# Kernel optimization log

Hardware: AMD Instinct MI355X
Metric: run time of the kernel (lower is better)

The kernel has to match this reference:

```python
import jax, jax.numpy as jnp
import numpy as np

N = 10000
E = 160000
H = 8
C = 128
D = 1024
NB = 3
NG = 64
NEG_SLOPE = 0.2
BN_EPS = 1e-5


def setup_inputs() -> dict:
    key = jax.random.key(0)
    ks = jax.random.split(key, 12)
    x = jax.random.normal(ks[0], (N, D), dtype=jnp.float32)
    edge_index = jax.random.randint(ks[1], (2, E), 0, N, dtype=jnp.int64)
    batch = jnp.sort(jax.random.randint(ks[2], (N,), 0, NG, dtype=jnp.int64))
    W = jax.random.normal(ks[3], (NB, D, D), dtype=jnp.float32) * 0.03
    att_src = jax.random.normal(ks[4], (NB, H, C), dtype=jnp.float32) * 0.1
    att_dst = jax.random.normal(ks[5], (NB, H, C), dtype=jnp.float32) * 0.1
    att_bias = jnp.zeros((NB, D), dtype=jnp.float32)
    gamma = jnp.ones((NB, D), dtype=jnp.float32)
    beta = jnp.zeros((NB, D), dtype=jnp.float32)
    W_out = jax.random.normal(ks[6], (D, 2), dtype=jnp.float32) * 0.03
    b_out = jnp.zeros((2,), dtype=jnp.float32)
    return {"x": x, "edge_index": edge_index, "batch": batch, "W": W,
            "att_src": att_src, "att_dst": att_dst, "att_bias": att_bias,
            "gamma": gamma, "beta": beta, "W_out": W_out, "b_out": b_out}


def _gat_conv(x, Wb, a_src, a_dst, bias, src, dst):
    # linear projection, per-head view: [N, H, C]
    h = (x @ Wb).reshape(N, H, C)
    alpha_src = jnp.einsum('nhc,hc->nh', h, a_src)  # [N,H]
    alpha_dst = jnp.einsum('nhc,hc->nh', h, a_dst)
    e = jax.nn.leaky_relu(alpha_src[src] + alpha_dst[dst], NEG_SLOPE)  # [Etot,H]
    # segment softmax over incoming edges per destination node
    m = jax.ops.segment_max(e, dst, num_segments=N)  # every node has self-loop
    ex = jnp.exp(e - m[dst])
    denom = jax.ops.segment_sum(ex, dst, num_segments=N)
    alpha = ex / denom[dst]  # [Etot,H]
    msg = alpha[:, :, None] * h[src]  # [Etot,H,C]
    out = jax.ops.segment_sum(msg, dst, num_segments=N).reshape(N, H * C)
    return out + bias


def _batchnorm(x, g, b):
    mu = jnp.mean(x, axis=0)
    var = jnp.mean(jnp.square(x - mu), axis=0)  # biased, training mode
    return (x - mu) * jax.lax.rsqrt(var + BN_EPS) * g + b


def reference(x, edge_index, batch, W, att_src, att_dst, att_bias, gamma, beta, W_out, b_out):
    # add self loops (PyG GATConv default)
    loop = jnp.arange(N, dtype=edge_index.dtype)
    src = jnp.concatenate([edge_index[0], loop])
    dst = jnp.concatenate([edge_index[1], loop])

    h = x
    prev = x
    for i in range(NB):
        att = _gat_conv(h, W[i], att_src[i], att_dst[i], att_bias[i], src, dst)
        o = jax.nn.relu(_batchnorm(prev + att, gamma[i], beta[i]))
        prev = h
        h = o

    # global mean pool over graphs
    sums = jax.ops.segment_sum(h, batch, num_segments=NG)
    cnts = jax.ops.segment_sum(jnp.ones((N,), dtype=h.dtype), batch, num_segments=NG)
    pooled = sums / jnp.maximum(cnts, 1.0)[:, None]
    return pooled @ W_out + b_out
```

## Files before the change

kernel.cpp:

```cpp
#include <hip/hip_runtime.h>
#include <hip/hip_bf16.h>

#define N_NODES 10000
#define E_EDGES 160000
#define ETOT    170000
#define H_HEADS 8
#define C_CH    128
#define D_DIM   1024
#define NBLK    3
#define NGRAPH  64
#define NEG_SLOPE 0.2f
#define BN_EPS  1e-5f

typedef __attribute__((ext_vector_type(8))) _Float16 half8;
typedef __attribute__((ext_vector_type(4))) _Float16 half4;
typedef __attribute__((ext_vector_type(2))) _Float16 half2v;
typedef __attribute__((ext_vector_type(4))) float f32x4;

__device__ inline int lower_bound_batch(const int* __restrict__ batch, int g) {
    int lo = 0, hi = N_NODES;
    while (lo < hi) {
        int mid = (lo + hi) >> 1;
        if (batch[mid] < g) lo = mid + 1;
        else hi = mid;
    }
    return lo;
}

__global__ void deg_kernel(const int* __restrict__ ei, int* __restrict__ deg) {
    int tid = blockIdx.x * blockDim.x + threadIdx.x;
    if (tid >= ETOT) return;
    int dst = (tid < E_EDGES) ? ei[E_EDGES + tid] : (tid - E_EDGES);
    atomicAdd(&deg[dst], 1);
}

__global__ void scan_kernel(const int* __restrict__ deg, int* __restrict__ ioff) {
    __shared__ int part[256];
    int t = threadIdx.x;
    const int CH = (N_NODES + 255) / 256;
    int base = t * CH;
    int s = 0;
    for (int j = 0; j < CH; ++j) {
        int idx = base + j;
        if (idx < N_NODES) s += deg[idx];
    }
    part[t] = s;
    __syncthreads();
    for (int o = 1; o < 256; o <<= 1) {
        int v = 0;
        if (t >= o) v = part[t - o];
        __syncthreads();
        part[t] += v;
        __syncthreads();
    }
    int run = (t == 0) ? 0 : part[t - 1];
    for (int j = 0; j < CH; ++j) {
        int idx = base + j;
        if (idx < N_NODES) { ioff[idx] = run; run += deg[idx]; }
    }
}

__global__ void scatter_kernel(const int* __restrict__ ei, int* __restrict__ ioff,
                               int* __restrict__ csr_src) {
    int tid = blockIdx.x * blockDim.x + threadIdx.x;
    if (tid >= ETOT) return;
    int src, dst;
    if (tid < E_EDGES) { src = ei[tid]; dst = ei[E_EDGES + tid]; }
    else { src = dst = tid - E_EDGES; }
    int pos = atomicAdd(&ioff[dst], 1);
    csr_src[pos] = src;
}

__global__ __launch_bounds__(256) void xconv_kernel(const float* __restrict__ in,
                                                    _Float16* __restrict__ o, int n4) {
    int i = blockIdx.x * blockDim.x + threadIdx.x;
    if (i >= n4) return;
    float4 v = ((const float4*)in)[i];
    half4 h = {(_Float16)v.x, (_Float16)v.y, (_Float16)v.z, (_Float16)v.w};
    ((half4*)o)[i] = h;
}

__global__ __launch_bounds__(256) void wtconv_kernel(const float* __restrict__ Wall,
                                                     _Float16* __restrict__ t16all) {
    const float* W = Wall + (size_t)blockIdx.z * D_DIM * D_DIM;
    _Float16* t16 = t16all + (size_t)blockIdx.z * D_DIM * D_DIM;
    __shared__ float t[32][33];
    int bn = blockIdx.x * 32;
    int bk = blockIdx.y * 32;
    int tx = threadIdx.x & 31;
    int ty = threadIdx.x >> 5;
#pragma unroll
    for (int r = 0; r < 32; r += 8)
        t[ty + r][tx] = W[(size_t)(bk + ty + r) * D_DIM + bn + tx];
    __syncthreads();
#pragma unroll
    for (int r = 0; r < 32; r += 8)
        t16[(size_t)(bn + ty + r) * D_DIM + bk + tx] = (_Float16)t[tx][ty + r];
}

__global__ __launch_bounds__(256) void gemm_mfma_kernel(const _Float16* __restrict__ A,
                                                        const _Float16* __restrict__ Bt,
                                                        _Float16* __restrict__ Hout,
                                                        const float* __restrict__ att_s,
                                                        const float* __restrict__ att_d,
                                                        float* __restrict__ asrc,
                                                        float* __restrict__ adst, int M) {
    __shared__ short As[128 * 32];
    __shared__ short Bs[128 * 32];
    __shared__ float sA[128], sD[128];
    int bm = blockIdx.y * 128;
    int bn = blockIdx.x * 128;
    int head = blockIdx.x;
    int tid = threadIdx.x;
    int wave = tid >> 6;
    int lane = tid & 63;
    int wm = (wave >> 1) * 64;
    int wn = (wave & 1) * 64;
    int quad = lane >> 4;
    int l16 = lane & 15;

    f32x4 acc[4][4];
#pragma unroll
    for (int i = 0; i < 4; ++i)
#pragma unroll
        for (int j = 0; j < 4; ++j) acc[i][j] = (f32x4){0.f, 0.f, 0.f, 0.f};

    int srow = lane >> 2;
    int scol = (lane & 3) * 16;

    for (int kb = 0; kb < 32; ++kb) {
        int k0 = kb * 32;
#pragma unroll
        for (int r = 0; r < 2; ++r) {
            int arow = wave * 16 + r * 64 + srow;
            int grow = bm + arow;
            if (grow > M - 1) grow = M - 1;
            const char* gp = (const char*)(A + (size_t)grow * 1024 + k0) + scol;
            __builtin_amdgcn_global_load_lds(
                (const __attribute__((address_space(1))) void*)gp,
                (__attribute__((address_space(3))) void*)((char*)As + (wave * 16 + r * 64) * 64),
                16, 0, 0);
        }
#pragma unroll
        for (int r = 0; r < 2; ++r) {
            int brow = wave * 16 + r * 64 + srow;
            const char* gp = (const char*)(Bt + (size_t)(bn + brow) * 1024 + k0) + scol;
            __builtin_amdgcn_global_load_lds(
                (const __attribute__((address_space(1))) void*)gp,
                (__attribute__((address_space(3))) void*)((char*)Bs + (wave * 16 + r * 64) * 64),
                16, 0, 0);
        }
        __syncthreads();

        half8 af[4], bfr[4];
#pragma unroll
        for (int i = 0; i < 4; ++i)
            af[i] = *(const half8*)(As + (wm + i * 16 + l16) * 32 + quad * 8);
#pragma unroll
        for (int j = 0; j < 4; ++j)
            bfr[j] = *(const half8*)(Bs + (wn + j * 16 + l16) * 32 + quad * 8);
#pragma unroll
        for (int i = 0; i < 4; ++i)
#pragma unroll
            for (int j = 0; j < 4; ++j)
                acc[i][j] = __builtin_amdgcn_mfma_f32_16x16x32_f16(af[i], bfr[j], acc[i][j], 0, 0, 0);
        __syncthreads();
    }

    float wsv[4], wdv[4];
#pragma unroll
    for (int j = 0; j < 4; ++j) {
        int c = wn + j * 16 + l16;
        wsv[j] = att_s[head * 128 + c];
        wdv[j] = att_d[head * 128 + c];
    }
    float psv[4][4], pdv[4][4];
#pragma unroll
    for (int i = 0; i < 4; ++i) {
#pragma unroll
        for (int reg = 0; reg < 4; ++reg) {
            float p = acc[i][0][reg] * wsv[0] + acc[i][1][reg] * wsv[1] +
                      acc[i][2][reg] * wsv[2] + acc[i][3][reg] * wsv[3];
            float q = acc[i][0][reg] * wdv[0] + acc[i][1][reg] * wdv[1] +
                      acc[i][2][reg] * wdv[2] + acc[i][3][reg] * wdv[3];
#pragma unroll
            for (int o = 1; o < 16; o <<= 1) {
                p += __shfl_xor(p, o);
                q += __shfl_xor(q, o);
            }
            psv[i][reg] = p;
            pdv[i][reg] = q;
        }
    }
    if ((wave & 1) == 0 && l16 == 0) {
#pragma unroll
        for (int i = 0; i < 4; ++i)
#pragma unroll
            for (int reg = 0; reg < 4; ++reg) {
                int r = wm + i * 16 + quad * 4 + reg;
                sA[r] = psv[i][reg];
                sD[r] = pdv[i][reg];
            }
    }
#pragma unroll
    for (int i = 0; i < 4; ++i) {
#pragma unroll
        for (int reg = 0; reg < 4; ++reg) {
            int gr = bm + wm + i * 16 + quad * 4 + reg;
            if (gr < M) {
                _Float16* hp = Hout + (size_t)head * N_NODES * 128 + (size_t)gr * 128 + wn + l16;
#pragma unroll
                for (int j = 0; j < 4; ++j) hp[j * 16] = (_Float16)acc[i][j][reg];
            }
        }
    }
    __syncthreads();
    if ((wave & 1) == 1 && l16 == 0) {
#pragma unroll
        for (int i = 0; i < 4; ++i)
#pragma unroll
            for (int reg = 0; reg < 4; ++reg) {
                int r = wm + i * 16 + quad * 4 + reg;
                int gr = bm + r;
                if (gr < M) {
                    asrc[gr * 8 + head] = sA[r] + psv[i][reg];
                    adst[gr * 8 + head] = sD[r] + pdv[i][reg];
                }
            }
    }
}

__global__ __launch_bounds__(256) void agg_kernel(const _Float16* __restrict__ h16,
                                                  const float* __restrict__ asrc,
                                                  const float* __restrict__ adst,
                                                  const int* __restrict__ ioff,
                                                  const int* __restrict__ csr_src,
                                                  const _Float16* __restrict__ prevh,
                                                  const float* __restrict__ bias,
                                                  _Float16* __restrict__ yout,
                                                  float* __restrict__ stats) {
    int bx = blockIdx.x;
    int tid = threadIdx.x;
    if (bx == 0) {
#pragma unroll
        for (int j = 0; j < 8; ++j) stats[tid + j * 256] = 0.f;
    }
    int head = bx & 7;
    int chunk = bx >> 3;
    int sub = tid >> 5;
    int lane = tid & 31;
    int n = chunk * 8 + sub;
    int c4 = lane * 4;
    const _Float16* hh = h16 + (size_t)head * N_NODES * 128;
    int start = (n == 0) ? 0 : ioff[n - 1];
    int end = ioff[n];
    float ad = adst[n * 8 + head];
    float den = 0.f;
    float4 acc = make_float4(0.f, 0.f, 0.f, 0.f);
    int p = start;
    for (; p + 4 <= end; p += 4) {
        int s0 = csr_src[p + 0];
        int s1 = csr_src[p + 1];
        int s2 = csr_src[p + 2];
        int s3 = csr_src[p + 3];
        float a0 = asrc[s0 * 8 + head];
        float a1 = asrc[s1 * 8 + head];
        float a2 = asrc[s2 * 8 + head];
        float a3 = asrc[s3 * 8 + head];
        half4 h0 = *(const half4*)(hh + (size_t)s0 * 128 + c4);
        half4 h1 = *(const half4*)(hh + (size_t)s1 * 128 + c4);
        half4 h2 = *(const half4*)(hh + (size_t)s2 * 128 + c4);
        half4 h3 = *(const half4*)(hh + (size_t)s3 * 128 + c4);
        float e0 = a0 + ad; e0 = (e0 > 0.f) ? e0 : NEG_SLOPE * e0;
        float e1 = a1 + ad; e1 = (e1 > 0.f) ? e1 : NEG_SLOPE * e1;
        float e2 = a2 + ad; e2 = (e2 > 0.f) ? e2 : NEG_SLOPE * e2;
        float e3 = a3 + ad; e3 = (e3 > 0.f) ? e3 : NEG_SLOPE * e3;
        float x0 = __expf(e0), x1 = __expf(e1), x2 = __expf(e2), x3 = __expf(e3);
        den += (x0 + x1) + (x2 + x3);
        acc.x += x0 * (float)h0[0] + x1 * (float)h1[0] + x2 * (float)h2[0] + x3 * (float)h3[0];
        acc.y += x0 * (float)h0[1] + x1 * (float)h1[1] + x2 * (float)h2[1] + x3 * (float)h3[1];
        acc.z += x0 * (float)h0[2] + x1 * (float)h1[2] + x2 * (float)h2[2] + x3 * (float)h3[2];
        acc.w += x0 * (float)h0[3] + x1 * (float)h1[3] + x2 * (float)h2[3] + x3 * (float)h3[3];
    }
    for (; p < end; ++p) {
        int s = csr_src[p];
        float e = asrc[s * 8 + head] + ad;
        e = (e > 0.f) ? e : NEG_SLOPE * e;
        float ex = __expf(e);
        den += ex;
        half4 hv = *(const half4*)(hh + (size_t)s * 128 + c4);
        acc.x = fmaf(ex, (float)hv[0], acc.x);
        acc.y = fmaf(ex, (float)hv[1], acc.y);
        acc.z = fmaf(ex, (float)hv[2], acc.z);
        acc.w = fmaf(ex, (float)hv[3], acc.w);
    }
    float invd = 1.0f / den;
    int col = head * 128 + c4;
    half4 ph = *(const half4*)(prevh + (size_t)n * 1024 + col);
    float4 bv = *(const float4*)(bias + col);
    float r0 = fmaf(acc.x, invd, (float)ph[0] + bv.x);
    float r1 = fmaf(acc.y, invd, (float)ph[1] + bv.y);
    float r2 = fmaf(acc.z, invd, (float)ph[2] + bv.z);
    float r3 = fmaf(acc.w, invd, (float)ph[3] + bv.w);
    half4 o = {(_Float16)r0, (_Float16)r1, (_Float16)r2, (_Float16)r3};
    *(half4*)(yout + (size_t)n * 1024 + col) = o;
}

__global__ void bn_stats_kernel(const _Float16* __restrict__ y, float* __restrict__ stats) {
    int col = (blockIdx.x * 256 + threadIdx.x) * 2;
    float s0 = 0.f, s1 = 0.f, q0 = 0.f, q1 = 0.f;
    for (int r = blockIdx.y; r < N_NODES; r += gridDim.y) {
        half2v v = *(const half2v*)(y + (size_t)r * 1024 + col);
        float a = (float)v[0], b = (float)v[1];
        s0 += a; q0 += a * a;
        s1 += b; q1 += b * b;
    }
    atomicAdd(&stats[col], s0);
    atomicAdd(&stats[col + 1], s1);
    atomicAdd(&stats[1024 + col], q0);
    atomicAdd(&stats[1024 + col + 1], q1);
}

__global__ void bn_apply_kernel(const _Float16* __restrict__ y, const float* __restrict__ stats,
                                const float* __restrict__ gamma, const float* __restrict__ beta,
                                _Float16* __restrict__ oout) {
    int idx4 = blockIdx.x * blockDim.x + threadIdx.x;
    if (idx4 >= N_NODES * D_DIM / 4) return;
    int base = idx4 * 4;
    int col = base & 1023;
    const float invN = 1.0f / (float)N_NODES;
    half4 v = ((const half4*)y)[idx4];
    float r[4];
#pragma unroll
    for (int j = 0; j < 4; ++j) {
        int cc = col + j;
        float mu = stats[cc] * invN;
        float var = stats[1024 + cc] * invN - mu * mu;
        float t = ((float)v[j] - mu) * rsqrtf(var + BN_EPS) * gamma[cc] + beta[cc];
        r[j] = fmaxf(t, 0.f);
    }
    half4 h = {(_Float16)r[0], (_Float16)r[1], (_Float16)r[2], (_Float16)r[3]};
    ((half4*)oout)[idx4] = h;
}

__global__ __launch_bounds__(256) void pool_kernel(const _Float16* __restrict__ h3,
                                                   const int* __restrict__ batch,
                                                   float* __restrict__ pooled) {
    int col = blockIdx.x * 256 + threadIdx.x;
    int g = blockIdx.y;
    int lo = lower_bound_batch(batch, g);
    int hi = lower_bound_batch(batch, g + 1);
    float acc = 0.f;
    for (int r = lo; r < hi; ++r) acc += (float)h3[(size_t)r * 1024 + col];
    pooled[(size_t)g * 1024 + col] = acc;
}

__global__ void final_kernel(const float* __restrict__ pooled, const int* __restrict__ batch,
                             const float* __restrict__ Wout, const float* __restrict__ bout,
                             float* __restrict__ out) {
    int g = blockIdx.x;
    int t = threadIdx.x;
    float p0 = 0.f, p1 = 0.f;
    for (int d = t; d < 1024; d += 256) {
        float v = pooled[(size_t)g * 1024 + d];
        p0 = fmaf(v, Wout[2 * d], p0);
        p1 = fmaf(v, Wout[2 * d + 1], p1);
    }
    __shared__ float s0[256], s1[256];
    s0[t] = p0; s1[t] = p1;
    __syncthreads();
    for (int o = 128; o; o >>= 1) {
        if (t < o) { s0[t] += s0[t + o]; s1[t] += s1[t + o]; }
        __syncthreads();
    }
    if (t == 0) {
        int cnt = lower_bound_batch(batch, g + 1) - lower_bound_batch(batch, g);
        float inv = 1.0f / fmaxf((float)cnt, 1.0f);
        out[g * 2 + 0] = s0[0] * inv + bout[0];
        out[g * 2 + 1] = s1[0] * inv + bout[1];
    }
}

extern "C" void kernel_launch(void* const* d_in, const int* in_sizes, int n_in,
                              void* d_out, int out_size, void* d_ws, size_t ws_size,
                              hipStream_t stream) {
    const float* x        = (const float*)d_in[0];
    const int*   ei       = (const int*)d_in[1];
    const int*   batch    = (const int*)d_in[2];
    const float* W        = (const float*)d_in[3];
    const float* att_src  = (const float*)d_in[4];
    const float* att_dst  = (const float*)d_in[5];
    const float* att_bias = (const float*)d_in[6];
    const float* gamma    = (const float*)d_in[7];
    const float* beta     = (const float*)d_in[8];
    const float* Wout     = (const float*)d_in[9];
    const float* bout     = (const float*)d_in[10];
    float* out = (float*)d_out;

    const size_t ND = (size_t)N_NODES * D_DIM;
    float* ws = (float*)d_ws;
    float* asrc   = ws;
    float* adst   = asrc + (size_t)N_NODES * H_HEADS;
    float* stats  = adst + (size_t)N_NODES * H_HEADS;
    float* pooled = stats + 2 * D_DIM;
    int* ideg     = (int*)(pooled + (size_t)NGRAPH * D_DIM);
    int* ioff     = ideg + N_NODES;
    int* csr_src  = ioff + N_NODES;
    _Float16* bufP  = (_Float16*)(csr_src + ETOT);
    _Float16* bufO0 = bufP + ND;
    _Float16* h16   = bufO0 + ND;
    _Float16* y16   = h16 + ND;
    _Float16* Wt3   = y16 + ND;

    hipMemsetAsync(ideg, 0, N_NODES * sizeof(int), stream);
    deg_kernel<<<(ETOT + 255) / 256, 256, 0, stream>>>(ei, ideg);
    scan_kernel<<<1, 256, 0, stream>>>(ideg, ioff);
    scatter_kernel<<<(ETOT + 255) / 256, 256, 0, stream>>>(ei, ioff, csr_src);
    xconv_kernel<<<(int)(ND / 4 + 255) / 256, 256, 0, stream>>>(x, bufP, (int)(ND / 4));
    wtconv_kernel<<<dim3(32, 32, 3), 256, 0, stream>>>(W, Wt3);

    const _Float16* Ain[3]  = {bufP, bufO0, bufP};
    const _Float16* Pin[3]  = {bufP, bufP, bufO0};
    _Float16* Oout[3]       = {bufO0, bufP, bufP};

    for (int i = 0; i < NBLK; ++i) {
        gemm_mfma_kernel<<<dim3(8, 79), 256, 0, stream>>>(
            Ain[i], Wt3 + (size_t)i * D_DIM * D_DIM, h16,
            att_src + i * H_HEADS * C_CH, att_dst + i * H_HEADS * C_CH,
            asrc, adst, N_NODES);
        agg_kernel<<<N_NODES, 256, 0, stream>>>(h16, asrc, adst, ioff, csr_src,
                                                Pin[i], att_bias + i * D_DIM, y16, stats);
        bn_stats_kernel<<<dim3(2, 128), 256, 0, stream>>>(y16, stats);
        bn_apply_kernel<<<(int)(ND / 4 + 255) / 256, 256, 0, stream>>>(
            y16, stats, gamma + i * D_DIM, beta + i * D_DIM, Oout[i]);
    }

    pool_kernel<<<dim3(4, NGRAPH), 256, 0, stream>>>(bufP, batch, pooled);
    final_kernel<<<NGRAPH, 256, 0, stream>>>(pooled, batch, Wout, bout, out);
}
```

Measured before the change: 625.0 us.

## Fuse BN statistics into aggregation, merge pooling kernels, remap GEMM grid by head

BatchNorm sum and sum-of-squares are now accumulated in the aggregation epilogue with a cross-lane shuffle and atomics, so the separate bn_stats pass over y16 is gone. Zeroing of stats moves into the GEMM kernel. The GEMM grid becomes 1-D with blocks grouped so eight consecutive M tiles share a head, which may improve L2 reuse of weights. Pool and final projection are merged into one kernel. The cost is many more atomics, roughly 10000 blocks × 32 lanes × 8 per layer, which could contend.

```diff
diff --git a/kernel.cpp b/kernel.cpp
--- a/kernel.cpp
+++ b/kernel.cpp
@@ -104,14 +104,23 @@
                                                         const float* __restrict__ att_s,
                                                         const float* __restrict__ att_d,
                                                         float* __restrict__ asrc,
-                                                        float* __restrict__ adst, int M) {
+                                                        float* __restrict__ adst,
+                                                        float* __restrict__ stats, int M) {
     __shared__ short As[128 * 32];
     __shared__ short Bs[128 * 32];
     __shared__ float sA[128], sD[128];
-    int bm = blockIdx.y * 128;
-    int bn = blockIdx.x * 128;
-    int head = blockIdx.x;
+    int bx = blockIdx.x;
     int tid = threadIdx.x;
+    if (bx == 0) {
+#pragma unroll
+        for (int j = 0; j < 8; ++j) stats[tid + j * 256] = 0.f;
+    }
+    int c = bx & 7;
+    int head = (bx >> 3) & 7;
+    int mt = c + 8 * (bx >> 6);
+    if (mt >= 79) return;
+    int bm = mt * 128;
+    int bn = head * 128;
     int wave = tid >> 6;
     int lane = tid & 63;
     int wm = (wave >> 1) * 64;
@@ -170,9 +179,9 @@
     float wsv[4], wdv[4];
 #pragma unroll
     for (int j = 0; j < 4; ++j) {
-        int c = wn + j * 16 + l16;
-        wsv[j] = att_s[head * 128 + c];
-        wdv[j] = att_d[head * 128 + c];
+        int cc = wn + j * 16 + l16;
+        wsv[j] = att_s[head * 128 + cc];
+        wdv[j] = att_d[head * 128 + cc];
     }
     float psv[4][4], pdv[4][4];
 #pragma unroll
@@ -241,10 +250,6 @@
                                                   float* __restrict__ stats) {
     int bx = blockIdx.x;
     int tid = threadIdx.x;
-    if (bx == 0) {
-#pragma unroll
-        for (int j = 0; j < 8; ++j) stats[tid + j * 256] = 0.f;
-    }
     int head = bx & 7;
     int chunk = bx >> 3;
     int sub = tid >> 5;
@@ -304,21 +309,18 @@
     float r3 = fmaf(acc.w, invd, (float)ph[3] + bv.w);
     half4 o = {(_Float16)r0, (_Float16)r1, (_Float16)r2, (_Float16)r3};
     *(half4*)(yout + (size_t)n * 1024 + col) = o;
-}
-
-__global__ void bn_stats_kernel(const _Float16* __restrict__ y, float* __restrict__ stats) {
-    int col = (blockIdx.x * 256 + threadIdx.x) * 2;
-    float s0 = 0.f, s1 = 0.f, q0 = 0.f, q1 = 0.f;
-    for (int r = blockIdx.y; r < N_NODES; r += gridDim.y) {
-        half2v v = *(const half2v*)(y + (size_t)r * 1024 + col);
-        float a = (float)v[0], b = (float)v[1];
-        s0 += a; q0 += a * a;
-        s1 += b; q1 += b * b;
-    }
-    atomicAdd(&stats[col], s0);
-    atomicAdd(&stats[col + 1], s1);
-    atomicAdd(&stats[1024 + col], q0);
-    atomicAdd(&stats[1024 + col + 1], q1);
+    float q0 = (float)o[0], q1 = (float)o[1], q2 = (float)o[2], q3 = (float)o[3];
+    float t0 = q0 * q0, t1 = q1 * q1, t2 = q2 * q2, t3 = q3 * q3;
+    q0 += __shfl_xor(q0, 32); t0 += __shfl_xor(t0, 32);
+    q1 += __shfl_xor(q1, 32); t1 += __shfl_xor(t1, 32);
+    q2 += __shfl_xor(q2, 32); t2 += __shfl_xor(t2, 32);
+    q3 += __shfl_xor(q3, 32); t3 += __shfl_xor(t3, 32);
+    if ((tid & 63) < 32) {
+        atomicAdd(&stats[col + 0], q0); atomicAdd(&stats[1024 + col + 0], t0);
+        atomicAdd(&stats[col + 1], q1); atomicAdd(&stats[1024 + col + 1], t1);
+        atomicAdd(&stats[col + 2], q2); atomicAdd(&stats[1024 + col + 2], t2);
+        atomicAdd(&stats[col + 3], q3); atomicAdd(&stats[1024 + col + 3], t3);
+    }
 }
 
 __global__ void bn_apply_kernel(const _Float16* __restrict__ y, const float* __restrict__ stats,
@@ -343,29 +345,25 @@
     ((half4*)oout)[idx4] = h;
 }
 
-__global__ __launch_bounds__(256) void pool_kernel(const _Float16* __restrict__ h3,
-                                                   const int* __restrict__ batch,
-                                                   float* __restrict__ pooled) {
-    int col = blockIdx.x * 256 + threadIdx.x;
-    int g = blockIdx.y;
+__global__ __launch_bounds__(256) void poolfinal_kernel(const _Float16* __restrict__ h3,
+                                                        const int* __restrict__ batch,
+                                                        const float* __restrict__ Wout,
+                                                        const float* __restrict__ bout,
+                                                        float* __restrict__ out) {
+    int g = blockIdx.x;
+    int t = threadIdx.x;
+    int col = t * 4;
     int lo = lower_bound_batch(batch, g);
     int hi = lower_bound_batch(batch, g + 1);
-    float acc = 0.f;
-    for (int r = lo; r < hi; ++r) acc += (float)h3[(size_t)r * 1024 + col];
-    pooled[(size_t)g * 1024 + col] = acc;
-}
-
-__global__ void final_kernel(const float* __restrict__ pooled, const int* __restrict__ batch,
-                             const float* __restrict__ Wout, const float* __restrict__ bout,
-                             float* __restrict__ out) {
-    int g = blockIdx.x;
-    int t = threadIdx.x;
-    float p0 = 0.f, p1 = 0.f;
-    for (int d = t; d < 1024; d += 256) {
-        float v = pooled[(size_t)g * 1024 + d];
-        p0 = fmaf(v, Wout[2 * d], p0);
-        p1 = fmaf(v, Wout[2 * d + 1], p1);
-    }
+    float a0 = 0.f, a1 = 0.f, a2 = 0.f, a3 = 0.f;
+    for (int r = lo; r < hi; ++r) {
+        half4 v = *(const half4*)(h3 + (size_t)r * 1024 + col);
+        a0 += (float)v[0]; a1 += (float)v[1]; a2 += (float)v[2]; a3 += (float)v[3];
+    }
+    float p0 = a0 * Wout[2 * col] + a1 * Wout[2 * (col + 1)] +
+               a2 * Wout[2 * (col + 2)] + a3 * Wout[2 * (col + 3)];
+    float p1 = a0 * Wout[2 * col + 1] + a1 * Wout[2 * (col + 1) + 1] +
+               a2 * Wout[2 * (col + 2) + 1] + a3 * Wout[2 * (col + 3) + 1];
     __shared__ float s0[256], s1[256];
     s0[t] = p0; s1[t] = p1;
     __syncthreads();
@@ -374,8 +372,7 @@
         __syncthreads();
     }
     if (t == 0) {
-        int cnt = lower_bound_batch(batch, g + 1) - lower_bound_batch(batch, g);
-        float inv = 1.0f / fmaxf((float)cnt, 1.0f);
+        float inv = 1.0f / fmaxf((float)(hi - lo), 1.0f);
         out[g * 2 + 0] = s0[0] * inv + bout[0];
         out[g * 2 + 1] = s1[0] * inv + bout[1];
     }
@@ -402,8 +399,7 @@
     float* asrc   = ws;
     float* adst   = asrc + (size_t)N_NODES * H_HEADS;
     float* stats  = adst + (size_t)N_NODES * H_HEADS;
-    float* pooled = stats + 2 * D_DIM;
-    int* ideg     = (int*)(pooled + (size_t)NGRAPH * D_DIM);
+    int* ideg     = (int*)(stats + 2 * D_DIM);
     int* ioff     = ideg + N_NODES;
     int* csr_src  = ioff + N_NODES;
     _Float16* bufP  = (_Float16*)(csr_src + ETOT);
@@ -424,17 +420,15 @@
     _Float16* Oout[3]       = {bufO0, bufP, bufP};
 
     for (int i = 0; i < NBLK; ++i) {
-        gemm_mfma_kernel<<<dim3(8, 79), 256, 0, stream>>>(
+        gemm_mfma_kernel<<<640, 256, 0, stream>>>(
             Ain[i], Wt3 + (size_t)i * D_DIM * D_DIM, h16,
             att_src + i * H_HEADS * C_CH, att_dst + i * H_HEADS * C_CH,
-            asrc, adst, N_NODES);
+            asrc, adst, stats, N_NODES);
         agg_kernel<<<N_NODES, 256, 0, stream>>>(h16, asrc, adst, ioff, csr_src,
                                                 Pin[i], att_bias + i * D_DIM, y16, stats);
-        bn_stats_kernel<<<dim3(2, 128), 256, 0, stream>>>(y16, stats);
         bn_apply_kernel<<<(int)(ND / 4 + 255) / 256, 256, 0, stream>>>(
             y16, stats, gamma + i * D_DIM, beta + i * D_DIM, Oout[i]);
     }
 
-    pool_kernel<<<dim3(4, NGRAPH), 256, 0, stream>>>(bufP, batch, pooled);
-    final_kernel<<<NGRAPH, 256, 0, stream>>>(pooled, batch, Wout, bout, out);
-}
+    poolfinal_kernel<<<NGRAPH, 256, 0, stream>>>(bufP, batch, Wout, bout, out);
+}
```

Result: slower. 1.859 ms (+197.5%).
